# Kernel optimization log

Hardware: AMD Instinct MI355X
Metric: run time of the kernel (lower is better)

## Reference

```python
import jax, jax.numpy as jnp
import numpy as np

B, L, H, V, G, TGB = 128, 512, 256, 100000, 4, 128
S = 2 * L - 1  # max_sequence_tokens = 2*history_capacity - 1


def setup_inputs() -> dict:
    key = jax.random.key(0)
    ks = jax.random.split(key, 16)
    d = {}
    d['history_tokens'] = jax.random.randint(ks[0], (B, L), 0, V)
    d['history_post_tokens'] = jax.random.randint(ks[1], (B, L), 0, V)
    d['history_author_tokens'] = jax.random.randint(ks[2], (B, L), 0, V)
    d['history_action_tokens'] = jax.random.randint(ks[3], (B, L), 0, V)
    d['history_time_gap'] = jax.random.randint(ks[4], (B, L), 0, TGB + 1)
    d['history_group_ids'] = jnp.sort(jax.random.randint(ks[5], (B, L), 0, G + 1), axis=-1)
    d['lengths'] = jax.random.randint(ks[6], (B,), 0, L + 1)
    # embedding tables (padding_idx=0 rows zeroed as in nn.Embedding(padding_idx=0))
    d['token_table'] = (jax.random.normal(ks[7], (V, H)) * 0.02).at[0].set(0.0)
    d['time_table'] = (jax.random.normal(ks[8], (TGB + 1, H)) * 0.02).at[0].set(0.0)
    d['group_table'] = (jax.random.normal(ks[9], (G + 1, H)) * 0.02).at[0].set(0.0)
    d['pos_table'] = jax.random.normal(ks[10], (S, H)) * 0.02
    d['sep_token'] = jax.random.normal(ks[11], (H,)) * 0.02
    # event_projection params: LayerNorm(6H) -> Linear(6H,4H) -> SiLU -> Linear(4H,H)
    d['ln_gamma'] = jnp.ones((6 * H,), jnp.float32)
    d['ln_beta'] = jnp.zeros((6 * H,), jnp.float32)
    d['W1'] = jax.random.normal(ks[12], (6 * H, 4 * H)) * (1.0 / np.sqrt(6 * H))
    d['b1'] = jnp.zeros((4 * H,), jnp.float32)
    d['W2'] = jax.random.normal(ks[13], (4 * H, H)) * (1.0 / np.sqrt(4 * H))
    d['b2'] = jnp.zeros((H,), jnp.float32)
    return d


def _layernorm(x, g, b, eps=1e-5):
    m = x.mean(-1, keepdims=True)
    v = x.var(-1, keepdims=True)
    return (x - m) / jnp.sqrt(v + eps) * g + b


def reference(history_tokens, history_post_tokens, history_author_tokens,
              history_action_tokens, history_time_gap, history_group_ids,
              lengths, token_table, time_table, group_table, pos_table,
              sep_token, ln_gamma, ln_beta, W1, b1, W2, b2):
    # --- event embedding: 6 lookups concat -> LN -> MLP  (dropout is eval no-op)
    ev = jnp.concatenate([
        token_table[history_tokens],
        token_table[history_post_tokens],
        token_table[history_author_tokens],
        token_table[history_action_tokens],
        time_table[jnp.clip(history_time_gap, 0, TGB)],
        group_table[history_group_ids],
    ], axis=-1)  # [B, L, 6H]
    h = _layernorm(ev, ln_gamma, ln_beta)
    h = jax.nn.silu(h @ W1 + b1)
    event = h @ W2 + b2  # [B, L, H]

    # --- vectorized merge_with_sep (ragged right-aligned pack with sep at group boundaries)
    pos = jnp.arange(L)
    mask = pos[None, :] < lengths[:, None]                       # prefix validity mask
    gid_next = jnp.concatenate([history_group_ids[:, 1:], history_group_ids[:, -1:]], axis=1)
    boundary = (pos[None, :] < lengths[:, None] - 1) & (history_group_ids != gid_next)
    ex = jnp.cumsum(boundary, axis=1) - boundary                 # seps strictly before event p
    event_idx = pos[None, :] + ex                                # piece index of event p
    M = lengths + boundary.sum(axis=1)                           # total pieces per row
    shift = S - M                                                # may be negative (left-truncate)
    pos_e = shift[:, None] + event_idx
    pos_s = pos_e + 1
    valid_e = mask & (pos_e >= 0)
    valid_s = boundary & (pos_s >= 0)
    barange = jnp.arange(B)[:, None]
    buf = jnp.zeros((B, S + 1, H), event.dtype)                  # extra slot S = trash bin
    buf = buf.at[barange, jnp.where(valid_e, pos_e, S)].set(
        jnp.where(valid_e[..., None], event, 0.0))
    buf = buf.at[barange, jnp.where(valid_s, pos_s, S)].set(
        jnp.where(valid_s[..., None], sep_token, 0.0))
    merged = buf[:, :S]
    merged_mask = jnp.arange(S)[None, :] >= jnp.maximum(shift, 0)[:, None]
    merged = (merged + pos_table[None]) * merged_mask[..., None].astype(merged.dtype)
    return merged, merged_mask
```

## Files before the change

kernel.cpp:

```cpp
#include <hip/hip_runtime.h>

#define B_    128
#define L_    512
#define H_    256
#define TGB_  128
#define S_    1023
#define BL_   (B_ * L_)
#define SIXH  1536
#define FOURH 1024

typedef __bf16 bf16_t;
typedef bf16_t bf16x8 __attribute__((ext_vector_type(8)));
typedef float  f32x4  __attribute__((ext_vector_type(4)));
typedef unsigned short u16x4 __attribute__((ext_vector_type(4)));

template<int P> struct IC { static constexpr int v = P; };

__device__ __forceinline__ unsigned short f2bf(float f) {
    union { float f; unsigned u; } v; v.f = f;
    unsigned u = v.u;
    unsigned r = u + 0x7FFFu + ((u >> 16) & 1u);
    return (unsigned short)(r >> 16);
}

__device__ __forceinline__ void gload_lds16(const void* g, void* l) {
    __builtin_amdgcn_global_load_lds(
        (__attribute__((address_space(1))) void*)(void*)(g),
        (__attribute__((address_space(3))) void*)(l), 16, 0, 0);
}

__global__ __launch_bounds__(256) void embed_ln_kernel(
    const int* __restrict__ tok,  const int* __restrict__ ptok,
    const int* __restrict__ atok, const int* __restrict__ actok,
    const int* __restrict__ tgap, const int* __restrict__ gid,
    const float* __restrict__ ttab, const float* __restrict__ titab,
    const float* __restrict__ gtab, const float* __restrict__ gamma,
    const float* __restrict__ beta, const int* __restrict__ row_id,
    const int* __restrict__ Vdev, unsigned short* __restrict__ xln)
{
    int j = blockIdx.x * 4 + (threadIdx.x >> 6);
    if (j >= *Vdev) return;
    int l = threadIdx.x & 63;
    int rid = row_id[j];
    int i0 = tok[rid], i1 = ptok[rid], i2 = atok[rid], i3 = actok[rid];
    int i4 = tgap[rid]; i4 = i4 < 0 ? 0 : (i4 > TGB_ ? TGB_ : i4);
    int i5 = gid[rid];
    f32x4 v[6];
    v[0] = *(const f32x4*)(ttab  + (size_t)i0 * H_ + l * 4);
    v[1] = *(const f32x4*)(ttab  + (size_t)i1 * H_ + l * 4);
    v[2] = *(const f32x4*)(ttab  + (size_t)i2 * H_ + l * 4);
    v[3] = *(const f32x4*)(ttab  + (size_t)i3 * H_ + l * 4);
    v[4] = *(const f32x4*)(titab + (size_t)i4 * H_ + l * 4);
    v[5] = *(const f32x4*)(gtab  + (size_t)i5 * H_ + l * 4);
    float s = 0.0f, sq = 0.0f;
    #pragma unroll
    for (int k = 0; k < 6; ++k)
        #pragma unroll
        for (int c = 0; c < 4; ++c) { float f = v[k][c]; s += f; sq += f * f; }
    #pragma unroll
    for (int off = 32; off > 0; off >>= 1) {
        s  += __shfl_xor(s,  off);
        sq += __shfl_xor(sq, off);
    }
    float mean = s * (1.0f / 1536.0f);
    float var  = sq * (1.0f / 1536.0f) - mean * mean;
    float rstd = rsqrtf(var + 1e-5f);
    unsigned short* orow = xln + (size_t)j * SIXH;
    #pragma unroll
    for (int k = 0; k < 6; ++k) {
        f32x4 g = *(const f32x4*)(gamma + k * H_ + l * 4);
        f32x4 b = *(const f32x4*)(beta  + k * H_ + l * 4);
        u16x4 o;
        #pragma unroll
        for (int c = 0; c < 4; ++c)
            o[c] = f2bf((v[k][c] - mean) * rstd * g[c] + b[c]);
        *(u16x4*)(orow + k * H_ + l * 4) = o;
    }
}

template<int K, int NTN, int EPI>
__global__ __launch_bounds__(256, 2) void gemm128_kernel(
    const unsigned short* __restrict__ A,
    const unsigned short* __restrict__ Bt,
    const float* __restrict__ bias,
    unsigned short* __restrict__ C,
    const int* __restrict__ outslot,
    const int* __restrict__ posC,
    const float* __restrict__ ptab,
    float* __restrict__ outF,
    const int* __restrict__ Vdev,
    const int* __restrict__ idx_map,
    const int* __restrict__ shiftb,
    const float* __restrict__ sep)
{
    constexpr int N = NTN * 128;
    constexpr int NT = K / 64;
    constexpr int IT = NT / 2;
    extern __shared__ __align__(16) unsigned short lds[];

    const int V = *Vdev;
    const int nact = ((V + 127) >> 7) * NTN;
    const int q = nact >> 3, r = nact & 7;

    const int t = threadIdx.x;
    const int w = t >> 6, l = t & 63;
    const int wm = w >> 1, wn = w & 1;
    const int r16 = l & 15, ql = l >> 4;
    const int sg = (t & 3) ^ ((t >> 3) & 3);
    unsigned short* ldsb = lds + w * 512;
    const int fr = (ql ^ ((r16 >> 1) & 3)) * 8;

    const unsigned short* la0 = lds + (wm * 64 + r16) * 32 + fr;
    const unsigned short* la1 = la0 + 16384;
    const unsigned short* lb0 = lds + 8192 + (wn * 64 + r16) * 32 + fr;
    const unsigned short* lb1 = lb0 + 16384;

    for (int bidv = blockIdx.x; bidv < nact; bidv += 512) {
        const int x = bidv & 7, o = bidv >> 3;
        const int wid = (x < r ? x * (q + 1) : r * (q + 1) + (x - r) * q) + o;
        const int mt  = wid / NTN;
        const int m0  = mt * 128;
        const int n0  = (wid - mt * NTN) * 128;

        const unsigned short* As0 = A  + (size_t)(m0 + (t >> 2)) * K + sg * 8;
        const unsigned short* As1 = As0 + (size_t)64 * K;
        const unsigned short* Bs0 = Bt + (size_t)(n0 + (t >> 2)) * K + sg * 8;
        const unsigned short* Bs1 = Bs0 + (size_t)64 * K;

        f32x4 acc[4][4];
        #pragma unroll
        for (int i = 0; i < 4; ++i)
            #pragma unroll
            for (int j = 0; j < 4; ++j) acc[i][j] = (f32x4)0.0f;

        auto ST2 = [&](const unsigned short* s0, const unsigned short* s1,
                       int dofs, int gofs) {
            gload_lds16(s0 + gofs, ldsb + dofs);
            gload_lds16(s1 + gofs, ldsb + dofs + 2048);
        };

        if (bidv != (int)blockIdx.x) __syncthreads();

        ST2(As0, As1, 0,     0);
        ST2(Bs0, Bs1, 8192,  0);
        ST2(As0, As1, 4096,  32);
        ST2(Bs0, Bs1, 12288, 32);
        ST2(As0, As1, 16384, 64);
        ST2(Bs0, Bs1, 24576, 64);
        asm volatile("s_waitcnt vmcnt(4)\ns_barrier" ::: "memory");

        bf16x8 bq[4];

        auto phase = [&](auto pc, bool last) {
            constexpr int P   = decltype(pc)::v;
            constexpr int BUF = P >> 2;
            constexpr int KK  = (P & 3) >> 1;
            constexpr int MH  = P & 1;
            const unsigned short* ab = (BUF ? la1 : la0) + KK * 4096 + MH * 1024;
            bf16x8 aq[2];
            if constexpr (MH == 0) {
                const unsigned short* bb = (BUF ? lb1 : lb0) + KK * 4096;
                bq[0] = *(const bf16x8*)(bb);
                bq[1] = *(const bf16x8*)(bb + 512);
                bq[2] = *(const bf16x8*)(bb + 1024);
                bq[3] = *(const bf16x8*)(bb + 1536);
            }
            aq[0] = *(const bf16x8*)(ab);
            aq[1] = *(const bf16x8*)(ab + 512);
            if constexpr (P == 0)      {            ST2(As0, As1, 20480, 96);  }
            else if constexpr (P == 1) {            ST2(Bs0, Bs1, 28672, 96);  }
            else if constexpr (P == 2) { if (!last) ST2(As0, As1, 0,     128); }
            else if constexpr (P == 3) { if (!last) ST2(Bs0, Bs1, 8192,  128); }
            else if constexpr (P == 4) { if (!last) ST2(As0, As1, 4096,  160); }
            else if constexpr (P == 5) { if (!last) ST2(Bs0, Bs1, 12288, 160); }
            else if constexpr (P == 6) { if (!last) ST2(As0, As1, 16384, 192); }
            else                       { if (!last) ST2(Bs0, Bs1, 24576, 192); }
            asm volatile("s_barrier" ::: "memory");
            __builtin_amdgcn_s_setprio(1);
            #pragma unroll
            for (int mm = 0; mm < 2; ++mm)
                #pragma unroll
                for (int nn = 0; nn < 4; ++nn)
                    acc[MH * 2 + mm][nn] = __builtin_amdgcn_mfma_f32_16x16x32_bf16(
                        aq[mm], bq[nn], acc[MH * 2 + mm][nn], 0, 0, 0);
            __builtin_amdgcn_s_setprio(0);
            if constexpr (P == 3) {
                if (last) asm volatile("s_waitcnt vmcnt(0)\ns_barrier" ::: "memory");
                else      asm volatile("s_waitcnt vmcnt(4)\ns_barrier" ::: "memory");
            } else if constexpr (P == 7) {
                if (!last) asm volatile("s_waitcnt vmcnt(4)\ns_barrier" ::: "memory");
            } else {
                asm volatile("s_barrier" ::: "memory");
            }
        };

        for (int it = 0; it < IT; ++it) {
            const bool last = (it == IT - 1);
            phase(IC<0>{}, last);
            phase(IC<1>{}, last);
            phase(IC<2>{}, last);
            phase(IC<3>{}, last);
            phase(IC<4>{}, last);
            phase(IC<5>{}, last);
            phase(IC<6>{}, last);
            phase(IC<7>{}, last);
            As0 += 128; As1 += 128; Bs0 += 128; Bs1 += 128;
        }

        if constexpr (EPI == 0) {
            #pragma unroll
            for (int mi = 0; mi < 4; ++mi) {
                #pragma unroll
                for (int ni = 0; ni < 4; ++ni) {
                    int col = n0 + wn * 64 + ni * 16 + r16;
                    float bv = bias[col];
                    #pragma unroll
                    for (int j = 0; j < 4; ++j) {
                        int row = m0 + wm * 64 + mi * 16 + ql * 4 + j;
                        float v = acc[mi][ni][j] + bv;
                        v = v / (1.0f + __expf(-v));
                        C[(size_t)row * N + col] = f2bf(v);
                    }
                }
            }
        } else {
            #pragma unroll
            for (int mi = 0; mi < 4; ++mi) {
                #pragma unroll
                for (int j = 0; j < 4; ++j) {
                    int row = m0 + wm * 64 + mi * 16 + ql * 4 + j;
                    int slot = outslot[row];
                    if (slot >= 0) {
                        float* orow = outF + (size_t)slot * H_;
                        const float* prow = ptab + (size_t)posC[row] * H_;
                        #pragma unroll
                        for (int ni = 0; ni < 4; ++ni) {
                            int col = n0 + wn * 64 + ni * 16 + r16;
                            orow[col] = acc[mi][ni][j] + bias[col] + prow[col];
                        }
                    }
                }
            }
        }
    }

    if constexpr (EPI == 2) {
        int hh = (t & 63) * 4;
        for (int u = blockIdx.x; u < 32768; u += 512) {
            int b = u >> 8;
            int s = (u & 255) * 4 + (t >> 6);
            if (s < S_) {
                int shift = shiftb[b];
                float* orow = outF + ((size_t)b * S_ + s) * H_;
                if (s < shift) {
                    *(f32x4*)(orow + hh) = (f32x4)0.0f;
                } else {
                    int idx = idx_map[b * S_ + s];
                    if (idx == -2) {
                        f32x4 pv = *(const f32x4*)(ptab + (size_t)s * H_ + hh);
                        f32x4 sv = *(const f32x4*)(sep + hh);
                        *(f32x4*)(orow + hh) = pv + sv;
                    }
                }
                if ((t & 63) == 0)
                    outF[(size_t)B_ * S_ * H_ + (size_t)b * S_ + s] = (s >= shift) ? 1.0f : 0.0f;
            }
        }
    }
}

__global__ __launch_bounds__(512) void scan_transpose_kernel(
    const int* __restrict__ gid, const int* __restrict__ lengths,
    int* __restrict__ idx_map, int* __restrict__ shiftb,
    int* __restrict__ row_id, int* __restrict__ outslot,
    int* __restrict__ posC, int* __restrict__ Vdev,
    const float* __restrict__ W1, const float* __restrict__ W2,
    unsigned short* __restrict__ W1T, unsigned short* __restrict__ W2T)
{
    int blk = blockIdx.x, i = threadIdx.x;
    if (blk >= B_) {
        __shared__ float tile[2][32][33];
        int half = i >> 8;
        int t = i & 255;
        int tidx = (blk - B_) * 2 + half;
        const float* in; unsigned short* out; int R, C, rb, cb;
        if (tidx < 1536) {
            in = W1; out = W1T; R = SIXH; C = FOURH;
            rb = (tidx % 48) * 32; cb = (tidx / 48) * 32;
        } else {
            int u = tidx - 1536;
            in = W2; out = W2T; R = FOURH; C = H_;
            rb = (u % 32) * 32; cb = (u / 32) * 32;
        }
        int tx = t & 31, ty = t >> 5;
        #pragma unroll
        for (int d = 0; d < 32; d += 8)
            tile[half][ty + d][tx] = in[(size_t)(rb + ty + d) * C + cb + tx];
        __syncthreads();
        #pragma unroll
        for (int d = 0; d < 32; d += 8)
            out[(size_t)(cb + ty + d) * R + rb + tx] = f2bf(tile[half][tx][ty + d]);
        return;
    }
    int b = blk;
    __shared__ int slen[128];
    __shared__ int sres[2];
    if (i < 128) slen[i] = lengths[i];
    __syncthreads();
    if (i < 64) {
        int vpart = (i < b ? slen[i] : 0) + (i + 64 < b ? slen[i + 64] : 0);
        int vall  = slen[i] + slen[i + 64];
        #pragma unroll
        for (int off = 32; off > 0; off >>= 1) {
            vpart += __shfl_xor(vpart, off);
            vall  += __shfl_xor(vall,  off);
        }
        if (i == 0) { sres[0] = vpart; sres[1] = vall; }
    }
    int len = lengths[b];
    int g  = gid[b * L_ + i];
    int gn = (i < L_ - 1) ? gid[b * L_ + i + 1] : g;
    int bnd = (i < len - 1 && g != gn) ? 1 : 0;
    __shared__ int sc[512];
    sc[i] = bnd;
    __syncthreads();
    for (int off = 1; off < 512; off <<= 1) {
        int v = (i >= off) ? sc[i - off] : 0;
        __syncthreads();
        sc[i] += v;
        __syncthreads();
    }
    int incl  = sc[i];
    int total = sc[511];
    int ex = incl - bnd;
    int M = len + total;
    int shift = S_ - M;
    int pb = sres[0], V = sres[1];
    for (int s = i; s < S_; s += 512) idx_map[b * S_ + s] = -1;
    __syncthreads();
    if (i < len) {
        int p = shift + i + ex;
        idx_map[b * S_ + p] = i;
        if (bnd) idx_map[b * S_ + p + 1] = -2;
        int j = pb + i;
        row_id[j]  = b * L_ + i;
        outslot[j] = b * S_ + p;
        posC[j]    = p;
    }
    if (i == 0) shiftb[b] = shift;
    if (b == B_ - 1) {
        if (i == 0) *Vdev = V;
        if (i < 256) outslot[V + i] = -1;
    }
}

extern "C" void kernel_launch(void* const* d_in, const int* in_sizes, int n_in,
                              void* d_out, int out_size, void* d_ws, size_t ws_size,
                              hipStream_t stream)
{
    const int*   tok   = (const int*)d_in[0];
    const int*   ptok  = (const int*)d_in[1];
    const int*   atok  = (const int*)d_in[2];
    const int*   actok = (const int*)d_in[3];
    const int*   tgap  = (const int*)d_in[4];
    const int*   gid   = (const int*)d_in[5];
    const int*   lens  = (const int*)d_in[6];
    const float* ttab  = (const float*)d_in[7];
    const float* titab = (const float*)d_in[8];
    const float* gtab  = (const float*)d_in[9];
    const float* post  = (const float*)d_in[10];
    const float* sep   = (const float*)d_in[11];
    const float* gamma = (const float*)d_in[12];
    const float* beta  = (const float*)d_in[13];
    const float* W1    = (const float*)d_in[14];
    const float* b1    = (const float*)d_in[15];
    const float* W2    = (const float*)d_in[16];
    const float* b2    = (const float*)d_in[17];

    unsigned short* xln  = (unsigned short*)d_ws;
    unsigned short* hbuf = xln  + (size_t)BL_ * SIXH;
    unsigned short* W1T  = hbuf + (size_t)BL_ * FOURH;
    unsigned short* W2T  = W1T  + (size_t)FOURH * SIXH;
    int* idx_map = (int*)(W2T + (size_t)H_ * FOURH);
    int* shiftb  = idx_map + B_ * S_;
    int* Vdev    = shiftb + B_;
    int* row_id  = Vdev + 4;
    int* outslot = row_id + BL_;
    int* posC    = outslot + BL_ + 256;
    float* out   = (float*)d_out;

    constexpr int LDSG = 2 * 16384 * 2;
    (void)hipFuncSetAttribute((const void*)&gemm128_kernel<SIXH, 8, 0>,
                              hipFuncAttributeMaxDynamicSharedMemorySize, LDSG);
    (void)hipFuncSetAttribute((const void*)&gemm128_kernel<FOURH, 2, 2>,
                              hipFuncAttributeMaxDynamicSharedMemorySize, LDSG);

    scan_transpose_kernel<<<B_ + 896, 512, 0, stream>>>(
        gid, lens, idx_map, shiftb, row_id, outslot, posC, Vdev,
        W1, W2, W1T, W2T);

    embed_ln_kernel<<<BL_ / 4, 256, 0, stream>>>(tok, ptok, atok, actok, tgap, gid,
                                                 ttab, titab, gtab, gamma, beta,
                                                 row_id, Vdev, xln);

    gemm128_kernel<SIXH, 8, 0><<<512, 256, LDSG, stream>>>(
        xln, W1T, b1, hbuf, nullptr, nullptr, nullptr, nullptr, Vdev,
        nullptr, nullptr, nullptr);
    gemm128_kernel<FOURH, 2, 2><<<512, 256, LDSG, stream>>>(
        hbuf, W2T, b2, nullptr, outslot, posC, post, out, Vdev,
        idx_map, shiftb, sep);
}
```

Measured before the change: 275.9 us.

## Fuse scan, weight transpose and embed-LN into one kernel; add atomic tile scheduler

Merges the scan/transpose kernel and the embedding+LayerNorm kernel into a single launch. Embedding blocks compute their own compacted row offset from lengths instead of waiting for row_id from the scan. This removes one launch and the dependency between the two. Both GEMMs switch from a static grid-stride tile loop to dynamic work stealing through an atomic counter in the workspace, which is zeroed by the pre-kernel, to balance uneven tile costs. The cost is an extra atomic plus barrier per tile.

```diff
diff --git a/kernel.cpp b/kernel.cpp
--- a/kernel.cpp
+++ b/kernel.cpp
@@ -29,52 +29,146 @@
         (__attribute__((address_space(3))) void*)(l), 16, 0, 0);
 }
 
-__global__ __launch_bounds__(256) void embed_ln_kernel(
+__global__ __launch_bounds__(512) void pre_kernel(
     const int* __restrict__ tok,  const int* __restrict__ ptok,
     const int* __restrict__ atok, const int* __restrict__ actok,
     const int* __restrict__ tgap, const int* __restrict__ gid,
+    const int* __restrict__ lengths,
     const float* __restrict__ ttab, const float* __restrict__ titab,
     const float* __restrict__ gtab, const float* __restrict__ gamma,
-    const float* __restrict__ beta, const int* __restrict__ row_id,
-    const int* __restrict__ Vdev, unsigned short* __restrict__ xln)
+    const float* __restrict__ beta,
+    const float* __restrict__ W1, const float* __restrict__ W2,
+    unsigned short* __restrict__ W1T, unsigned short* __restrict__ W2T,
+    unsigned short* __restrict__ xln,
+    int* __restrict__ idx_map, int* __restrict__ shiftb,
+    int* __restrict__ outslot, int* __restrict__ posC,
+    int* __restrict__ Vdev, int* __restrict__ ctr)
 {
-    int j = blockIdx.x * 4 + (threadIdx.x >> 6);
-    if (j >= *Vdev) return;
-    int l = threadIdx.x & 63;
-    int rid = row_id[j];
-    int i0 = tok[rid], i1 = ptok[rid], i2 = atok[rid], i3 = actok[rid];
-    int i4 = tgap[rid]; i4 = i4 < 0 ? 0 : (i4 > TGB_ ? TGB_ : i4);
-    int i5 = gid[rid];
-    f32x4 v[6];
-    v[0] = *(const f32x4*)(ttab  + (size_t)i0 * H_ + l * 4);
-    v[1] = *(const f32x4*)(ttab  + (size_t)i1 * H_ + l * 4);
-    v[2] = *(const f32x4*)(ttab  + (size_t)i2 * H_ + l * 4);
-    v[3] = *(const f32x4*)(ttab  + (size_t)i3 * H_ + l * 4);
-    v[4] = *(const f32x4*)(titab + (size_t)i4 * H_ + l * 4);
-    v[5] = *(const f32x4*)(gtab  + (size_t)i5 * H_ + l * 4);
-    float s = 0.0f, sq = 0.0f;
-    #pragma unroll
-    for (int k = 0; k < 6; ++k)
-        #pragma unroll
-        for (int c = 0; c < 4; ++c) { float f = v[k][c]; s += f; sq += f * f; }
-    #pragma unroll
-    for (int off = 32; off > 0; off >>= 1) {
-        s  += __shfl_xor(s,  off);
-        sq += __shfl_xor(sq, off);
-    }
-    float mean = s * (1.0f / 1536.0f);
-    float var  = sq * (1.0f / 1536.0f) - mean * mean;
-    float rstd = rsqrtf(var + 1e-5f);
-    unsigned short* orow = xln + (size_t)j * SIXH;
-    #pragma unroll
-    for (int k = 0; k < 6; ++k) {
-        f32x4 g = *(const f32x4*)(gamma + k * H_ + l * 4);
-        f32x4 b = *(const f32x4*)(beta  + k * H_ + l * 4);
-        u16x4 o;
-        #pragma unroll
-        for (int c = 0; c < 4; ++c)
-            o[c] = f2bf((v[k][c] - mean) * rstd * g[c] + b[c]);
-        *(u16x4*)(orow + k * H_ + l * 4) = o;
+    int blk = blockIdx.x, i = threadIdx.x;
+
+    if (blk >= 1024) {
+        int eblk = blk - 1024;
+        int b = eblk >> 6;
+        int w = i >> 6, l = i & 63;
+        int ei = (eblk & 63) * 8 + w;
+        int len = lengths[b];
+        if (ei >= len) return;
+        int vpart = (l < b ? lengths[l] : 0) + (l + 64 < b ? lengths[l + 64] : 0);
+        #pragma unroll
+        for (int off = 32; off > 0; off >>= 1) vpart += __shfl_xor(vpart, off);
+        int j = vpart + ei;
+        int rid = b * L_ + ei;
+        int i0 = tok[rid], i1 = ptok[rid], i2 = atok[rid], i3 = actok[rid];
+        int i4 = tgap[rid]; i4 = i4 < 0 ? 0 : (i4 > TGB_ ? TGB_ : i4);
+        int i5 = gid[rid];
+        f32x4 v[6];
+        v[0] = *(const f32x4*)(ttab  + (size_t)i0 * H_ + l * 4);
+        v[1] = *(const f32x4*)(ttab  + (size_t)i1 * H_ + l * 4);
+        v[2] = *(const f32x4*)(ttab  + (size_t)i2 * H_ + l * 4);
+        v[3] = *(const f32x4*)(ttab  + (size_t)i3 * H_ + l * 4);
+        v[4] = *(const f32x4*)(titab + (size_t)i4 * H_ + l * 4);
+        v[5] = *(const f32x4*)(gtab  + (size_t)i5 * H_ + l * 4);
+        float s = 0.0f, sq = 0.0f;
+        #pragma unroll
+        for (int k = 0; k < 6; ++k)
+            #pragma unroll
+            for (int c = 0; c < 4; ++c) { float f = v[k][c]; s += f; sq += f * f; }
+        #pragma unroll
+        for (int off = 32; off > 0; off >>= 1) {
+            s  += __shfl_xor(s,  off);
+            sq += __shfl_xor(sq, off);
+        }
+        float mean = s * (1.0f / 1536.0f);
+        float var  = sq * (1.0f / 1536.0f) - mean * mean;
+        float rstd = rsqrtf(var + 1e-5f);
+        unsigned short* orow = xln + (size_t)j * SIXH;
+        #pragma unroll
+        for (int k = 0; k < 6; ++k) {
+            f32x4 g = *(const f32x4*)(gamma + k * H_ + l * 4);
+            f32x4 bb = *(const f32x4*)(beta + k * H_ + l * 4);
+            u16x4 o;
+            #pragma unroll
+            for (int c = 0; c < 4; ++c)
+                o[c] = f2bf((v[k][c] - mean) * rstd * g[c] + bb[c]);
+            *(u16x4*)(orow + k * H_ + l * 4) = o;
+        }
+        return;
+    }
+
+    if (blk >= B_) {
+        __shared__ float tile[2][32][33];
+        int half = i >> 8;
+        int t = i & 255;
+        int tidx = (blk - B_) * 2 + half;
+        const float* in; unsigned short* out; int R, C, rb, cb;
+        if (tidx < 1536) {
+            in = W1; out = W1T; R = SIXH; C = FOURH;
+            rb = (tidx % 48) * 32; cb = (tidx / 48) * 32;
+        } else {
+            int u = tidx - 1536;
+            in = W2; out = W2T; R = FOURH; C = H_;
+            rb = (u % 32) * 32; cb = (u / 32) * 32;
+        }
+        int tx = t & 31, ty = t >> 5;
+        #pragma unroll
+        for (int d = 0; d < 32; d += 8)
+            tile[half][ty + d][tx] = in[(size_t)(rb + ty + d) * C + cb + tx];
+        __syncthreads();
+        #pragma unroll
+        for (int d = 0; d < 32; d += 8)
+            out[(size_t)(cb + ty + d) * R + rb + tx] = f2bf(tile[half][tx][ty + d]);
+        return;
+    }
+
+    int b = blk;
+    if (b == 0 && i < 2) ctr[i] = 0;
+    __shared__ int slen[128];
+    __shared__ int sres[2];
+    if (i < 128) slen[i] = lengths[i];
+    __syncthreads();
+    if (i < 64) {
+        int vpart = (i < b ? slen[i] : 0) + (i + 64 < b ? slen[i + 64] : 0);
+        int vall  = slen[i] + slen[i + 64];
+        #pragma unroll
+        for (int off = 32; off > 0; off >>= 1) {
+            vpart += __shfl_xor(vpart, off);
+            vall  += __shfl_xor(vall,  off);
+        }
+        if (i == 0) { sres[0] = vpart; sres[1] = vall; }
+    }
+    int len = lengths[b];
+    int g  = gid[b * L_ + i];
+    int gn = (i < L_ - 1) ? gid[b * L_ + i + 1] : g;
+    int bnd = (i < len - 1 && g != gn) ? 1 : 0;
+    __shared__ int sc[512];
+    sc[i] = bnd;
+    __syncthreads();
+    for (int off = 1; off < 512; off <<= 1) {
+        int v = (i >= off) ? sc[i - off] : 0;
+        __syncthreads();
+        sc[i] += v;
+        __syncthreads();
+    }
+    int incl  = sc[i];
+    int total = sc[511];
+    int ex = incl - bnd;
+    int M = len + total;
+    int shift = S_ - M;
+    int pb = sres[0], V = sres[1];
+    for (int s = i; s < S_; s += 512) idx_map[b * S_ + s] = -1;
+    __syncthreads();
+    if (i < len) {
+        int p = shift + i + ex;
+        idx_map[b * S_ + p] = i;
+        if (bnd) idx_map[b * S_ + p + 1] = -2;
+        int j = pb + i;
+        outslot[j] = b * S_ + p;
+        posC[j]    = p;
+    }
+    if (i == 0) shiftb[b] = shift;
+    if (b == B_ - 1) {
+        if (i == 0) *Vdev = V;
+        if (i < 256) outslot[V + i] = -1;
     }
 }
 
@@ -91,7 +185,8 @@
     const int* __restrict__ Vdev,
     const int* __restrict__ idx_map,
     const int* __restrict__ shiftb,
-    const float* __restrict__ sep)
+    const float* __restrict__ sep,
+    int* __restrict__ ctr)
 {
     constexpr int N = NTN * 128;
     constexpr int NT = K / 64;
@@ -115,7 +210,9 @@
     const unsigned short* lb0 = lds + 8192 + (wn * 64 + r16) * 32 + fr;
     const unsigned short* lb1 = lb0 + 16384;
 
-    for (int bidv = blockIdx.x; bidv < nact; bidv += 512) {
+    __shared__ int snext;
+    bool first = true;
+    for (int bidv = blockIdx.x; bidv < nact; ) {
         const int x = bidv & 7, o = bidv >> 3;
         const int wid = (x < r ? x * (q + 1) : r * (q + 1) + (x - r) * q) + o;
         const int mt  = wid / NTN;
@@ -139,7 +236,8 @@
             gload_lds16(s1 + gofs, ldsb + dofs + 2048);
         };
 
-        if (bidv != (int)blockIdx.x) __syncthreads();
+        if (!first) __syncthreads();
+        first = false;
 
         ST2(As0, As1, 0,     0);
         ST2(Bs0, Bs1, 8192,  0);
@@ -242,6 +340,10 @@
                 }
             }
         }
+
+        if (t == 0) snext = 512 + atomicAdd(ctr, 1);
+        __syncthreads();
+        bidv = snext;
     }
 
     if constexpr (EPI == 2) {
@@ -266,91 +368,6 @@
                     outF[(size_t)B_ * S_ * H_ + (size_t)b * S_ + s] = (s >= shift) ? 1.0f : 0.0f;
             }
         }
-    }
-}
-
-__global__ __launch_bounds__(512) void scan_transpose_kernel(
-    const int* __restrict__ gid, const int* __restrict__ lengths,
-    int* __restrict__ idx_map, int* __restrict__ shiftb,
-    int* __restrict__ row_id, int* __restrict__ outslot,
-    int* __restrict__ posC, int* __restrict__ Vdev,
-    const float* __restrict__ W1, const float* __restrict__ W2,
-    unsigned short* __restrict__ W1T, unsigned short* __restrict__ W2T)
-{
-    int blk = blockIdx.x, i = threadIdx.x;
-    if (blk >= B_) {
-        __shared__ float tile[2][32][33];
-        int half = i >> 8;
-        int t = i & 255;
-        int tidx = (blk - B_) * 2 + half;
-        const float* in; unsigned short* out; int R, C, rb, cb;
-        if (tidx < 1536) {
-            in = W1; out = W1T; R = SIXH; C = FOURH;
-            rb = (tidx % 48) * 32; cb = (tidx / 48) * 32;
-        } else {
-            int u = tidx - 1536;
-            in = W2; out = W2T; R = FOURH; C = H_;
-            rb = (u % 32) * 32; cb = (u / 32) * 32;
-        }
-        int tx = t & 31, ty = t >> 5;
-        #pragma unroll
-        for (int d = 0; d < 32; d += 8)
-            tile[half][ty + d][tx] = in[(size_t)(rb + ty + d) * C + cb + tx];
-        __syncthreads();
-        #pragma unroll
-        for (int d = 0; d < 32; d += 8)
-            out[(size_t)(cb + ty + d) * R + rb + tx] = f2bf(tile[half][tx][ty + d]);
-        return;
-    }
-    int b = blk;
-    __shared__ int slen[128];
-    __shared__ int sres[2];
-    if (i < 128) slen[i] = lengths[i];
-    __syncthreads();
-    if (i < 64) {
-        int vpart = (i < b ? slen[i] : 0) + (i + 64 < b ? slen[i + 64] : 0);
-        int vall  = slen[i] + slen[i + 64];
-        #pragma unroll
-        for (int off = 32; off > 0; off >>= 1) {
-            vpart += __shfl_xor(vpart, off);
-            vall  += __shfl_xor(vall,  off);
-        }
-        if (i == 0) { sres[0] = vpart; sres[1] = vall; }
-    }
-    int len = lengths[b];
-    int g  = gid[b * L_ + i];
-    int gn = (i < L_ - 1) ? gid[b * L_ + i + 1] : g;
-    int bnd = (i < len - 1 && g != gn) ? 1 : 0;
-    __shared__ int sc[512];
-    sc[i] = bnd;
-    __syncthreads();
-    for (int off = 1; off < 512; off <<= 1) {
-        int v = (i >= off) ? sc[i - off] : 0;
-        __syncthreads();
-        sc[i] += v;
-        __syncthreads();
-    }
-    int incl  = sc[i];
-    int total = sc[511];
-    int ex = incl - bnd;
-    int M = len + total;
-    int shift = S_ - M;
-    int pb = sres[0], V = sres[1];
-    for (int s = i; s < S_; s += 512) idx_map[b * S_ + s] = -1;
-    __syncthreads();
-    if (i < len) {
-        int p = shift + i + ex;
-        idx_map[b * S_ + p] = i;
-        if (bnd) idx_map[b * S_ + p + 1] = -2;
-        int j = pb + i;
-        row_id[j]  = b * L_ + i;
-        outslot[j] = b * S_ + p;
-        posC[j]    = p;
-    }
-    if (i == 0) shiftb[b] = shift;
-    if (b == B_ - 1) {
-        if (i == 0) *Vdev = V;
-        if (i < 256) outslot[V + i] = -1;
     }
 }
 
@@ -384,9 +401,9 @@
     int* idx_map = (int*)(W2T + (size_t)H_ * FOURH);
     int* shiftb  = idx_map + B_ * S_;
     int* Vdev    = shiftb + B_;
-    int* row_id  = Vdev + 4;
-    int* outslot = row_id + BL_;
+    int* outslot = Vdev + 4;
     int* posC    = outslot + BL_ + 256;
+    int* ctr     = posC + BL_;
     float* out   = (float*)d_out;
 
     constexpr int LDSG = 2 * 16384 * 2;
@@ -395,18 +412,16 @@
     (void)hipFuncSetAttribute((const void*)&gemm128_kernel<FOURH, 2, 2>,
                               hipFuncAttributeMaxDynamicSharedMemorySize, LDSG);
 
-    scan_transpose_kernel<<<B_ + 896, 512, 0, stream>>>(
-        gid, lens, idx_map, shiftb, row_id, outslot, posC, Vdev,
-        W1, W2, W1T, W2T);
-
-    embed_ln_kernel<<<BL_ / 4, 256, 0, stream>>>(tok, ptok, atok, actok, tgap, gid,
-                                                 ttab, titab, gtab, gamma, beta,
-                                                 row_id, Vdev, xln);
+    pre_kernel<<<1024 + BL_ / 8, 512, 0, stream>>>(
+        tok, ptok, atok, actok, tgap, gid, lens,
+        ttab, titab, gtab, gamma, beta,
+        W1, W2, W1T, W2T, xln,
+        idx_map, shiftb, outslot, posC, Vdev, ctr);
 
     gemm128_kernel<SIXH, 8, 0><<<512, 256, LDSG, stream>>>(
         xln, W1T, b1, hbuf, nullptr, nullptr, nullptr, nullptr, Vdev,
-        nullptr, nullptr, nullptr);
+        nullptr, nullptr, nullptr, ctr);
     gemm128_kernel<FOURH, 2, 2><<<512, 256, LDSG, stream>>>(
         hbuf, W2T, b2, nullptr, outslot, posC, post, out, Vdev,
-        idx_map, shiftb, sep);
+        idx_map, shiftb, sep, ctr + 1);
 }
```

New measurement: 307.0 us. +11.3%, slower.
